# Kernel optimization log

Hardware: AMD Instinct MI355X
Metric: run time of the kernel (lower is better)

The kernel has to match this reference:

```python
import jax, jax.numpy as jnp
import numpy as np

B, T, D_MODEL, N_HEADS = 4, 2048, 1024, 16
D_K = D_MODEL // N_HEADS


def setup_inputs() -> dict:
    key = jax.random.key(0)
    kx, kq, kk, kv, ko = jax.random.split(key, 5)
    scale = 1.0 / np.sqrt(D_MODEL)  # ~ torch Linear init scale
    return {
        "x": jax.random.normal(kx, (B, T, D_MODEL), dtype=jnp.float32),
        "W_q": jax.random.uniform(kq, (D_MODEL, D_MODEL), jnp.float32, -scale, scale),
        "W_k": jax.random.uniform(kk, (D_MODEL, D_MODEL), jnp.float32, -scale, scale),
        "W_v": jax.random.uniform(kv, (D_MODEL, D_MODEL), jnp.float32, -scale, scale),
        "W_o": jax.random.uniform(ko, (D_MODEL, D_MODEL), jnp.float32, -scale, scale),
    }


def reference(x, W_q, W_k, W_v, W_o):
    b, t, _ = x.shape
    # nn.Linear(y) = y @ W.T ; split to (B, H, T, d_k)
    def split_heads(y):
        return y.reshape(b, t, N_HEADS, D_K).transpose(0, 2, 1, 3)

    Q = split_heads(x @ W_q.T)
    K = split_heads(x @ W_k.T)
    V = split_heads(x @ W_v.T)

    scores = jnp.einsum("bhqd,bhkd->bhqk", Q, K) / jnp.sqrt(jnp.float32(D_K))
    causal = jnp.triu(jnp.ones((t, t), dtype=bool), k=1)  # True = masked
    scores = jnp.where(causal, -jnp.inf, scores)
    weights = jax.nn.softmax(scores, axis=-1)
    out = jnp.einsum("bhqk,bhkd->bhqd", weights, V)
    out = out.transpose(0, 2, 1, 3).reshape(b, t, D_MODEL)
    return out @ W_o.T
```

## Files before the change

kernel.cpp:

```cpp
#include <hip/hip_runtime.h>

typedef __attribute__((ext_vector_type(8))) short s16x8;
typedef __attribute__((ext_vector_type(4))) float fx4;
typedef __attribute__((ext_vector_type(4))) int ix4;

#define B_SZ 4
#define T_SZ 2048
#define DM 1024
#define NH 16
#define DK 64
#define M_SZ (B_SZ * T_SZ)
#define NINF (-__builtin_inff())
#define QSCALE (0.125f * 1.44269504088896340736f)

__device__ __forceinline__ unsigned short f2bf(float f) {
    unsigned int u = __float_as_uint(f);
    unsigned int r = u + 0x7fffu + ((u >> 16) & 1u);
    return (unsigned short)(r >> 16);
}

__device__ __forceinline__ unsigned cvtpk(float lo, float hi) {
    unsigned r;
    asm("v_cvt_pk_bf16_f32 %0, %1, %2" : "=v"(r) : "v"(lo), "v"(hi));
    return r;
}

__device__ __forceinline__ void async16(const unsigned short* g, unsigned short* l) {
    __builtin_amdgcn_global_load_lds(
        (const __attribute__((address_space(1))) unsigned int*)g,
        (__attribute__((address_space(3))) unsigned int*)l, 16, 0, 0);
}

__global__ void cast_f32_bf16(const float* __restrict__ src, unsigned short* __restrict__ dst, int n) {
    int i = (blockIdx.x * blockDim.x + threadIdx.x) * 4;
    int stride = gridDim.x * blockDim.x * 4;
    for (; i + 3 < n; i += stride) {
        float4 v = *(const float4*)(src + i);
        ushort4 o;
        o.x = f2bf(v.x); o.y = f2bf(v.y); o.z = f2bf(v.z); o.w = f2bf(v.w);
        *(ushort4*)(dst + i) = o;
    }
}

__global__ void cast_w4(const float* __restrict__ s0, const float* __restrict__ s1,
                        const float* __restrict__ s2, const float* __restrict__ s3,
                        unsigned short* __restrict__ dst) {
    const float* s = (blockIdx.y == 0) ? s0 : (blockIdx.y == 1) ? s1 : (blockIdx.y == 2) ? s2 : s3;
    unsigned short* d = dst + (size_t)blockIdx.y * (DM * DM);
    int i = (blockIdx.x * blockDim.x + threadIdx.x) * 4;
    int stride = gridDim.x * blockDim.x * 4;
    for (; i + 3 < DM * DM; i += stride) {
        float4 v = *(const float4*)(s + i);
        ushort4 o;
        o.x = f2bf(v.x); o.y = f2bf(v.y); o.z = f2bf(v.z); o.w = f2bf(v.w);
        *(ushort4*)(d + i) = o;
    }
}

__global__ __launch_bounds__(512, 2) void gemm_qkv256(const unsigned short* __restrict__ A,
                                                      const unsigned short* __restrict__ W,
                                                      unsigned short* __restrict__ Qs,
                                                      unsigned short* __restrict__ Kb,
                                                      unsigned short* __restrict__ Vt) {
    __shared__ __align__(16) unsigned short S[49152];

    const int t = threadIdx.x;
    const int lane = t & 63, w = t >> 6;
    const int wm = w >> 2, wn = w & 3;
    const int lrow = lane & 15, lk = lane >> 4;
    const int bx = blockIdx.x;
    const int m0 = blockIdx.y * 128;
    const int K = DM;
    const int NKT = K / 64;

    fx4 acc[4][4] = {};

    const int srow = t >> 3;
    const int cs = (t & 7) ^ (srow & 7);
    const unsigned short* Ag = A + (long)(m0 + srow) * K + cs * 8;
    const unsigned short* Bg = W + (long)(bx * 256 + srow) * K + cs * 8;

    async16(Ag,           &S[t * 8]);
    async16(Ag + 64 * K,  &S[4096 + t * 8]);
    async16(Bg,           &S[16384 + t * 8]);
    async16(Bg + 64 * K,  &S[16384 + 4096 + t * 8]);
    async16(Bg + 128 * K, &S[16384 + 8192 + t * 8]);
    async16(Bg + 192 * K, &S[16384 + 12288 + t * 8]);
    asm volatile("s_waitcnt vmcnt(0)" ::: "memory");
    __syncthreads();

    for (int kt = 0; kt < NKT; ++kt) {
        const int cur = kt & 1;
        if (kt + 1 < NKT) {
            const int ko = (kt + 1) * 64;
            const int nbA = (cur ^ 1) * 8192;
            const int nbB = 16384 + (cur ^ 1) * 16384;
            async16(Ag + ko,           &S[nbA + t * 8]);
            async16(Ag + 64 * K + ko,  &S[nbA + 4096 + t * 8]);
            async16(Bg + ko,           &S[nbB + t * 8]);
            async16(Bg + 64 * K + ko,  &S[nbB + 4096 + t * 8]);
            async16(Bg + 128 * K + ko, &S[nbB + 8192 + t * 8]);
            async16(Bg + 192 * K + ko, &S[nbB + 12288 + t * 8]);
        }
        const unsigned short* Ab = &S[cur * 8192];
        const unsigned short* Bb = &S[16384 + cur * 16384];
#pragma unroll
        for (int kk = 0; kk < 2; ++kk) {
            const int sw = ((kk * 4 + lk) ^ (lrow & 7)) * 8;
            s16x8 af[4], bf[4];
#pragma unroll
            for (int mf = 0; mf < 4; ++mf)
                af[mf] = *(const s16x8*)&Ab[(wm * 64 + mf * 16 + lrow) * 64 + sw];
#pragma unroll
            for (int nf = 0; nf < 4; ++nf)
                bf[nf] = *(const s16x8*)&Bb[(wn * 64 + nf * 16 + lrow) * 64 + sw];
            __builtin_amdgcn_s_setprio(1);
#pragma unroll
            for (int mf = 0; mf < 4; ++mf)
#pragma unroll
                for (int nf = 0; nf < 4; ++nf)
                    acc[mf][nf] = __builtin_amdgcn_mfma_f32_16x16x32_bf16(af[mf], bf[nf], acc[mf][nf], 0, 0, 0);
            __builtin_amdgcn_s_setprio(0);
        }
        asm volatile("s_waitcnt vmcnt(0)" ::: "memory");
        __syncthreads();
    }

    const int which = bx >> 2;
    const int n0l = (bx & 3) * 256;
    if (which < 2) {
        unsigned short* dst = which ? Kb : Qs;
        const float sc = which ? 1.f : QSCALE;
#pragma unroll
        for (int mf = 0; mf < 4; ++mf)
#pragma unroll
            for (int nf = 0; nf < 4; ++nf)
#pragma unroll
                for (int r = 0; r < 4; ++r) {
                    int row = m0 + wm * 64 + mf * 16 + lk * 4 + r;
                    int col = n0l + wn * 64 + nf * 16 + lrow;
                    dst[(long)row * DM + col] = f2bf(acc[mf][nf][r] * sc);
                }
    } else {
#pragma unroll
        for (int mf = 0; mf < 4; ++mf)
#pragma unroll
            for (int nf = 0; nf < 4; ++nf) {
                const int cl = wn * 64 + nf * 16 + lrow;
                const int rl = wm * 64 + mf * 16 + lk * 4;
                ushort4 pk;
                pk.x = f2bf(acc[mf][nf][0]); pk.y = f2bf(acc[mf][nf][1]);
                pk.z = f2bf(acc[mf][nf][2]); pk.w = f2bf(acc[mf][nf][3]);
                *(ushort4*)&S[cl * 132 + rl] = pk;
            }
        __syncthreads();
        const int c = t >> 1, h2 = t & 1;
        unsigned short* vtp = Vt + (long)(n0l + c) * M_SZ + m0 + h2 * 64;
#pragma unroll
        for (int j = 0; j < 8; ++j) {
            union { struct { ushort4 a, b; } s; ix4 v; } u;
            u.s.a = *(const ushort4*)&S[c * 132 + h2 * 64 + j * 8];
            u.s.b = *(const ushort4*)&S[c * 132 + h2 * 64 + j * 8 + 4];
            *(ix4*)(vtp + j * 8) = u.v;
        }
    }
}

template<int OUT_BF16>
__global__ __launch_bounds__(256) void gemm_bt(const unsigned short* __restrict__ A,
                                               const unsigned short* __restrict__ Bw,
                                               void* __restrict__ Cout,
                                               int M, int N, int K, float scale) {
    __shared__ __align__(16) unsigned short As[2][128 * 32];
    __shared__ __align__(16) unsigned short Bs[2][128 * 32];

    const int t = threadIdx.x;
    const int lane = t & 63;
    const int w = t >> 6;
    const int wm = w >> 1, wn = w & 1;
    const int lrow = lane & 15, lk = lane >> 4;
    const int m0 = blockIdx.y * 128, n0 = blockIdx.x * 128;

    fx4 acc[4][4] = {};

    const int arow = t >> 2;
    const int acol = (t & 3) * 8;
    const unsigned short* Ag = A + (long)(m0 + arow) * K + acol;
    const unsigned short* Bg = Bw + (long)(n0 + arow) * K + acol;
    const int lds0 = t * 8;
    const int nk = K / 32;

    async16(Ag, &As[0][lds0]);
    async16(Ag + 64 * K, &As[0][lds0 + 64 * 32]);
    async16(Bg, &Bs[0][lds0]);
    async16(Bg + 64 * K, &Bs[0][lds0 + 64 * 32]);

    for (int kt = 0; kt < nk; ++kt) {
        const int cur = kt & 1;
        if (kt + 1 < nk) {
            const int ko = (kt + 1) * 32;
            async16(Ag + ko, &As[cur ^ 1][lds0]);
            async16(Ag + 64 * K + ko, &As[cur ^ 1][lds0 + 64 * 32]);
            async16(Bg + ko, &Bs[cur ^ 1][lds0]);
            async16(Bg + 64 * K + ko, &Bs[cur ^ 1][lds0 + 64 * 32]);
            asm volatile("s_waitcnt vmcnt(4)" ::: "memory");
        } else {
            asm volatile("s_waitcnt vmcnt(0)" ::: "memory");
        }
        __syncthreads();

        s16x8 af[4], bf[4];
#pragma unroll
        for (int i = 0; i < 4; ++i)
            af[i] = *(const s16x8*)&As[cur][(wm * 64 + i * 16 + lrow) * 32 + lk * 8];
#pragma unroll
        for (int i = 0; i < 4; ++i)
            bf[i] = *(const s16x8*)&Bs[cur][(wn * 64 + i * 16 + lrow) * 32 + lk * 8];
#pragma unroll
        for (int i = 0; i < 4; ++i)
#pragma unroll
            for (int j = 0; j < 4; ++j)
                acc[i][j] = __builtin_amdgcn_mfma_f32_16x16x32_bf16(af[i], bf[j], acc[i][j], 0, 0, 0);
        __syncthreads();
    }

#pragma unroll
    for (int i = 0; i < 4; ++i)
#pragma unroll
        for (int j = 0; j < 4; ++j)
#pragma unroll
            for (int r = 0; r < 4; ++r) {
                int row = m0 + wm * 64 + i * 16 + lk * 4 + r;
                int col = n0 + wn * 64 + j * 16 + lrow;
                float v = acc[i][j][r] * scale;
                if (OUT_BF16)
                    ((unsigned short*)Cout)[(long)row * N + col] = f2bf(v);
                else
                    ((float*)Cout)[(long)row * N + col] = v;
            }
}

__global__ __launch_bounds__(256, 4) void attn_kernel(const unsigned short* __restrict__ Q,
                                                      const unsigned short* __restrict__ Kb,
                                                      const unsigned short* __restrict__ Vt,
                                                      unsigned short* __restrict__ O) {
    __shared__ __align__(16) unsigned short Ks[2][64 * 64];
    __shared__ __align__(16) unsigned short Vs[2][64 * 64];
    __shared__ __align__(16) unsigned short Pl[4][16 * 72];

    const int t = threadIdx.x;
    const int lane = t & 63, w = t >> 6;
    const int lrow = lane & 15, lk = lane >> 4;
    const int hb = blockIdx.x;
    const int h = hb & 15, b = hb >> 4;
    const int qb = 15 - blockIdx.y;
    const int row0 = b * T_SZ;
    const int q0w = qb * 128 + w * 32;

    s16x8 qf[2][2];
#pragma unroll
    for (int hh = 0; hh < 2; ++hh) {
        const unsigned short* qp = Q + (long)(row0 + q0w + hh * 16 + lrow) * DM + h * DK + lk * 8;
        qf[hh][0] = *(const s16x8*)qp;
        qf[hh][1] = *(const s16x8*)(qp + 32);
    }

    fx4 acc[2][4] = {};
    float mrun[2] = {NINF, NINF}, lsum[2] = {0.f, 0.f};

    const int srow = t >> 3;
    const int chk = (t & 7) ^ (srow & 7);
    const unsigned short* Kg = Kb + (long)(row0 + srow) * DM + h * DK + chk * 8;
    const unsigned short* Vg = Vt + (long)(h * DK + srow) * M_SZ + row0 + chk * 8;
    unsigned short* Kl = &Ks[0][t * 8];
    unsigned short* Vl = &Vs[0][t * 8];

    const int nt = 2 * qb + 2;

    async16(Kg, Kl);
    async16(Kg + 32 * DM, Kl + 2048);
    async16(Vg, Vl);
    async16(Vg + 32 * (long)M_SZ, Vl + 2048);
    asm volatile("s_waitcnt vmcnt(0)" ::: "memory");
    __syncthreads();

    for (int kt = 0; kt < nt; ++kt) {
        const int cur = kt & 1;
        const bool pre = (kt + 1 < nt);
        if (pre) {
            const long koff = (long)(kt + 1) * 64 * DM;
            const int voff = (kt + 1) * 64;
            async16(Kg + koff, Kl + (cur ^ 1) * 4096);
            async16(Kg + koff + 32 * DM, Kl + (cur ^ 1) * 4096 + 2048);
            async16(Vg + voff, Vl + (cur ^ 1) * 4096);
            async16(Vg + voff + 32 * (long)M_SZ, Vl + (cur ^ 1) * 4096 + 2048);
        }
        const int kv0 = kt * 64;
        if (kv0 <= q0w + 31) {
            const char* ksb = (const char*)&Ks[cur][0];
            float p[2][4][4];
            float pm0 = NINF, pm1 = NINF;
#pragma unroll
            for (int sub = 0; sub < 4; ++sub) {
                const int kv0s = kv0 + sub * 16;
                if (kv0s <= q0w + 31) {
                    const int rb = (sub * 16 + lrow) << 7;
                    const int sw = (lrow & 7) << 4;
                    const s16x8 kf0 = *(const s16x8*)(ksb + (rb + ((lk * 16) ^ sw)));
                    const s16x8 kf1 = *(const s16x8*)(ksb + (rb + ((64 + lk * 16) ^ sw)));
                    fx4 s1 = {};
                    s1 = __builtin_amdgcn_mfma_f32_16x16x32_bf16(kf0, qf[1][0], s1, 0, 0, 0);
                    s1 = __builtin_amdgcn_mfma_f32_16x16x32_bf16(kf1, qf[1][1], s1, 0, 0, 0);
                    if (kv0s + 15 > q0w + 16) {
#pragma unroll
                        for (int r = 0; r < 4; ++r)
                            if (kv0s + lk * 4 + r > q0w + 16 + lrow) s1[r] = NINF;
                    }
#pragma unroll
                    for (int r = 0; r < 4; ++r) { p[1][sub][r] = s1[r]; pm1 = fmaxf(pm1, s1[r]); }
                    if (kv0s <= q0w + 15) {
                        fx4 s0 = {};
                        s0 = __builtin_amdgcn_mfma_f32_16x16x32_bf16(kf0, qf[0][0], s0, 0, 0, 0);
                        s0 = __builtin_amdgcn_mfma_f32_16x16x32_bf16(kf1, qf[0][1], s0, 0, 0, 0);
                        if (kv0s + 15 > q0w) {
#pragma unroll
                            for (int r = 0; r < 4; ++r)
                                if (kv0s + lk * 4 + r > q0w + lrow) s0[r] = NINF;
                        }
#pragma unroll
                        for (int r = 0; r < 4; ++r) { p[0][sub][r] = s0[r]; pm0 = fmaxf(pm0, s0[r]); }
                    } else {
#pragma unroll
                        for (int r = 0; r < 4; ++r) p[0][sub][r] = NINF;
                    }
                } else {
#pragma unroll
                    for (int r = 0; r < 4; ++r) { p[0][sub][r] = NINF; p[1][sub][r] = NINF; }
                }
            }
            float pmv[2] = {pm0, pm1};
#pragma unroll
            for (int hh = 0; hh < 2; ++hh) {
                float pm = pmv[hh];
                pm = fmaxf(pm, __shfl_xor(pm, 16));
                pm = fmaxf(pm, __shfl_xor(pm, 32));
                if (__any(pm > mrun[hh] + 8.f)) {
                    const float mnew = fmaxf(mrun[hh], pm);
                    const float sc = exp2f(mrun[hh] - mnew);
                    mrun[hh] = mnew;
                    lsum[hh] *= sc;
#pragma unroll
                    for (int r = 0; r < 4; ++r) {
                        const float scr = __shfl(sc, lk * 4 + r);
                        acc[hh][0][r] *= scr; acc[hh][1][r] *= scr;
                        acc[hh][2][r] *= scr; acc[hh][3][r] *= scr;
                    }
                }
                float ps = 0.f;
#pragma unroll
                for (int sub = 0; sub < 4; ++sub)
#pragma unroll
                    for (int r = 0; r < 4; ++r) {
                        const float pv = exp2f(p[hh][sub][r] - mrun[hh]);
                        p[hh][sub][r] = pv;
                        ps += pv;
                    }
                ps += __shfl_xor(ps, 16);
                ps += __shfl_xor(ps, 32);
                lsum[hh] += ps;
            }
            s16x8 pf[2][2];
#pragma unroll
            for (int hh = 0; hh < 2; ++hh) {
#pragma unroll
                for (int sub = 0; sub < 4; ++sub) {
                    uint2 pw;
                    pw.x = cvtpk(p[hh][sub][0], p[hh][sub][1]);
                    pw.y = cvtpk(p[hh][sub][2], p[hh][sub][3]);
                    *(uint2*)&Pl[w][lrow * 72 + sub * 16 + lk * 4] = pw;
                }
                pf[hh][0] = *(const s16x8*)&Pl[w][lrow * 72 + lk * 8];
                pf[hh][1] = *(const s16x8*)&Pl[w][lrow * 72 + 32 + lk * 8];
            }
#pragma unroll
            for (int s = 0; s < 2; ++s) {
                if (kv0 + s * 32 <= q0w + 31) {
                    const bool h0a = (kv0 + s * 32 <= q0w + 15);
#pragma unroll
                    for (int nf = 0; nf < 4; ++nf) {
                        const int d = nf * 16 + lrow;
                        const s16x8 vf = *(const s16x8*)&Vs[cur][d * 64 + (((s * 4 + lk) ^ (lrow & 7)) << 3)];
                        if (h0a)
                            acc[0][nf] = __builtin_amdgcn_mfma_f32_16x16x32_bf16(pf[0][s], vf, acc[0][nf], 0, 0, 0);
                        acc[1][nf] = __builtin_amdgcn_mfma_f32_16x16x32_bf16(pf[1][s], vf, acc[1][nf], 0, 0, 0);
                    }
                }
            }
        }
        asm volatile("s_waitcnt vmcnt(0)" ::: "memory");
        __syncthreads();
    }

#pragma unroll
    for (int hh = 0; hh < 2; ++hh) {
        float linv[4];
#pragma unroll
        for (int r = 0; r < 4; ++r) linv[r] = 1.f / __shfl(lsum[hh], lk * 4 + r);
        unsigned short* op = O + (long)(row0 + q0w + hh * 16) * DM + h * DK;
#pragma unroll
        for (int nf = 0; nf < 4; ++nf)
#pragma unroll
            for (int r = 0; r < 4; ++r)
                op[(long)(lk * 4 + r) * DM + nf * 16 + lrow] = f2bf(acc[hh][nf][r] * linv[r]);
    }
}

extern "C" void kernel_launch(void* const* d_in, const int* in_sizes, int n_in,
                              void* d_out, int out_size, void* d_ws, size_t ws_size,
                              hipStream_t stream) {
    const float* x  = (const float*)d_in[0];
    const float* Wq = (const float*)d_in[1];
    const float* Wk = (const float*)d_in[2];
    const float* Wv = (const float*)d_in[3];
    const float* Wo = (const float*)d_in[4];
    float* out = (float*)d_out;

    unsigned short* wsu = (unsigned short*)d_ws;
    unsigned short* xb  = wsu;
    unsigned short* wqb = xb + 8388608;
    unsigned short* wob = wqb + 3 * 1048576;
    unsigned short* Qs  = wob + 1048576;
    unsigned short* Ob  = Qs + 8388608;

    unsigned short* Kb = (unsigned short*)d_out;
    unsigned short* Vt = Kb + 8388608;

    cast_f32_bf16<<<2048, 256, 0, stream>>>(x, xb, M_SZ * DM);
    cast_w4<<<dim3(256, 4), 256, 0, stream>>>(Wq, Wk, Wv, Wo, wqb);

    gemm_qkv256<<<dim3(12, M_SZ / 128), 512, 0, stream>>>(xb, wqb, Qs, Kb, Vt);

    dim3 agrid(64, 16);
    attn_kernel<<<agrid, 256, 0, stream>>>(Qs, Kb, Vt, Ob);

    dim3 ggrid(DM / 128, M_SZ / 128);
    gemm_bt<0><<<ggrid, 256, 0, stream>>>(Ob, wob, out, M_SZ, DM, DM, 1.f);
}
```

Before: 198.9 us.

## Merge cast kernels, use 128x256 swizzled output GEMM, MFMA row sums in attention

Combines the x and weight cast kernels into one launch, cutting one kernel launch. Replaces the 128x128 output-projection GEMM with a 512-thread 128x256 tile that uses a K=64 step, XOR-swizzled LDS and s_setprio around the MFMA block, aiming for more reuse and fewer LDS bank conflicts. In attention, the softmax row-sum is computed by an MFMA against a ones vector instead of per-lane adds and shuffles, which adds MFMA work but removes the cross-lane reductions. The bf16 rounding of P now also enters the denominator, which slightly changes the numerics.

After: 201.0 us. Within noise of the previous version (+1.0%).

```diff
diff --git a/kernel.cpp b/kernel.cpp
--- a/kernel.cpp
+++ b/kernel.cpp
@@ -31,25 +31,23 @@
         (__attribute__((address_space(3))) unsigned int*)l, 16, 0, 0);
 }
 
-__global__ void cast_f32_bf16(const float* __restrict__ src, unsigned short* __restrict__ dst, int n) {
+__global__ void cast_all(const float* __restrict__ x,
+                         const float* __restrict__ s1, const float* __restrict__ s2,
+                         const float* __restrict__ s3, const float* __restrict__ s4,
+                         unsigned short* __restrict__ xb, unsigned short* __restrict__ wb) {
+    const int y = blockIdx.y;
+    const float* s;
+    unsigned short* d;
+    int n;
+    if (y == 0) { s = x; d = xb; n = M_SZ * DM; }
+    else {
+        s = (y == 1) ? s1 : (y == 2) ? s2 : (y == 3) ? s3 : s4;
+        d = wb + (size_t)(y - 1) * (DM * DM);
+        n = DM * DM;
+    }
     int i = (blockIdx.x * blockDim.x + threadIdx.x) * 4;
     int stride = gridDim.x * blockDim.x * 4;
     for (; i + 3 < n; i += stride) {
-        float4 v = *(const float4*)(src + i);
-        ushort4 o;
-        o.x = f2bf(v.x); o.y = f2bf(v.y); o.z = f2bf(v.z); o.w = f2bf(v.w);
-        *(ushort4*)(dst + i) = o;
-    }
-}
-
-__global__ void cast_w4(const float* __restrict__ s0, const float* __restrict__ s1,
-                        const float* __restrict__ s2, const float* __restrict__ s3,
-                        unsigned short* __restrict__ dst) {
-    const float* s = (blockIdx.y == 0) ? s0 : (blockIdx.y == 1) ? s1 : (blockIdx.y == 2) ? s2 : s3;
-    unsigned short* d = dst + (size_t)blockIdx.y * (DM * DM);
-    int i = (blockIdx.x * blockDim.x + threadIdx.x) * 4;
-    int stride = gridDim.x * blockDim.x * 4;
-    for (; i + 3 < DM * DM; i += stride) {
         float4 v = *(const float4*)(s + i);
         ushort4 o;
         o.x = f2bf(v.x); o.y = f2bf(v.y); o.z = f2bf(v.z); o.w = f2bf(v.w);
@@ -166,77 +164,82 @@
     }
 }
 
-template<int OUT_BF16>
-__global__ __launch_bounds__(256) void gemm_bt(const unsigned short* __restrict__ A,
-                                               const unsigned short* __restrict__ Bw,
-                                               void* __restrict__ Cout,
-                                               int M, int N, int K, float scale) {
-    __shared__ __align__(16) unsigned short As[2][128 * 32];
-    __shared__ __align__(16) unsigned short Bs[2][128 * 32];
+__global__ __launch_bounds__(512, 2) void gemm_out256(const unsigned short* __restrict__ A,
+                                                      const unsigned short* __restrict__ W,
+                                                      float* __restrict__ C) {
+    __shared__ __align__(16) unsigned short S[49152];
 
     const int t = threadIdx.x;
-    const int lane = t & 63;
-    const int w = t >> 6;
-    const int wm = w >> 1, wn = w & 1;
+    const int lane = t & 63, w = t >> 6;
+    const int wm = w >> 2, wn = w & 3;
     const int lrow = lane & 15, lk = lane >> 4;
-    const int m0 = blockIdx.y * 128, n0 = blockIdx.x * 128;
+    const int n0 = blockIdx.x * 256;
+    const int m0 = blockIdx.y * 128;
+    const int K = DM;
+    const int NKT = K / 64;
 
     fx4 acc[4][4] = {};
 
-    const int arow = t >> 2;
-    const int acol = (t & 3) * 8;
-    const unsigned short* Ag = A + (long)(m0 + arow) * K + acol;
-    const unsigned short* Bg = Bw + (long)(n0 + arow) * K + acol;
-    const int lds0 = t * 8;
-    const int nk = K / 32;
-
-    async16(Ag, &As[0][lds0]);
-    async16(Ag + 64 * K, &As[0][lds0 + 64 * 32]);
-    async16(Bg, &Bs[0][lds0]);
-    async16(Bg + 64 * K, &Bs[0][lds0 + 64 * 32]);
-
-    for (int kt = 0; kt < nk; ++kt) {
+    const int srow = t >> 3;
+    const int cs = (t & 7) ^ (srow & 7);
+    const unsigned short* Ag = A + (long)(m0 + srow) * K + cs * 8;
+    const unsigned short* Bg = W + (long)(n0 + srow) * K + cs * 8;
+
+    async16(Ag,           &S[t * 8]);
+    async16(Ag + 64 * K,  &S[4096 + t * 8]);
+    async16(Bg,           &S[16384 + t * 8]);
+    async16(Bg + 64 * K,  &S[16384 + 4096 + t * 8]);
+    async16(Bg + 128 * K, &S[16384 + 8192 + t * 8]);
+    async16(Bg + 192 * K, &S[16384 + 12288 + t * 8]);
+    asm volatile("s_waitcnt vmcnt(0)" ::: "memory");
+    __syncthreads();
+
+    for (int kt = 0; kt < NKT; ++kt) {
         const int cur = kt & 1;
-        if (kt + 1 < nk) {
-            const int ko = (kt + 1) * 32;
-            async16(Ag + ko, &As[cur ^ 1][lds0]);
-            async16(Ag + 64 * K + ko, &As[cur ^ 1][lds0 + 64 * 32]);
-            async16(Bg + ko, &Bs[cur ^ 1][lds0]);
-            async16(Bg + 64 * K + ko, &Bs[cur ^ 1][lds0 + 64 * 32]);
-            asm volatile("s_waitcnt vmcnt(4)" ::: "memory");
-        } else {
-            asm volatile("s_waitcnt vmcnt(0)" ::: "memory");
-        }
+        if (kt + 1 < NKT) {
+            const int ko = (kt + 1) * 64;
+            const int nbA = (cur ^ 1) * 8192;
+            const int nbB = 16384 + (cur ^ 1) * 16384;
+            async16(Ag + ko,           &S[nbA + t * 8]);
+            async16(Ag + 64 * K + ko,  &S[nbA + 4096 + t * 8]);
+            async16(Bg + ko,           &S[nbB + t * 8]);
+            async16(Bg + 64 * K + ko,  &S[nbB + 4096 + t * 8]);
+            async16(Bg + 128 * K + ko, &S[nbB + 8192 + t * 8]);
+            async16(Bg + 192 * K + ko, &S[nbB + 12288 + t * 8]);
+        }
+        const unsigned short* Ab = &S[cur * 8192];
+        const unsigned short* Bb = &S[16384 + cur * 16384];
+#pragma unroll
+        for (int kk = 0; kk < 2; ++kk) {
+            const int sw = ((kk * 4 + lk) ^ (lrow & 7)) * 8;
+            s16x8 af[4], bf[4];
+#pragma unroll
+            for (int mf = 0; mf < 4; ++mf)
+                af[mf] = *(const s16x8*)&Ab[(wm * 64 + mf * 16 + lrow) * 64 + sw];
+#pragma unroll
+            for (int nf = 0; nf < 4; ++nf)
+                bf[nf] = *(const s16x8*)&Bb[(wn * 64 + nf * 16 + lrow) * 64 + sw];
+            __builtin_amdgcn_s_setprio(1);
+#pragma unroll
+            for (int mf = 0; mf < 4; ++mf)
+#pragma unroll
+                for (int nf = 0; nf < 4; ++nf)
+                    acc[mf][nf] = __builtin_amdgcn_mfma_f32_16x16x32_bf16(af[mf], bf[nf], acc[mf][nf], 0, 0, 0);
+            __builtin_amdgcn_s_setprio(0);
+        }
+        asm volatile("s_waitcnt vmcnt(0)" ::: "memory");
         __syncthreads();
-
-        s16x8 af[4], bf[4];
-#pragma unroll
-        for (int i = 0; i < 4; ++i)
-            af[i] = *(const s16x8*)&As[cur][(wm * 64 + i * 16 + lrow) * 32 + lk * 8];
-#pragma unroll
-        for (int i = 0; i < 4; ++i)
-            bf[i] = *(const s16x8*)&Bs[cur][(wn * 64 + i * 16 + lrow) * 32 + lk * 8];
-#pragma unroll
-        for (int i = 0; i < 4; ++i)
-#pragma unroll
-            for (int j = 0; j < 4; ++j)
-                acc[i][j] = __builtin_amdgcn_mfma_f32_16x16x32_bf16(af[i], bf[j], acc[i][j], 0, 0, 0);
-        __syncthreads();
-    }
-
-#pragma unroll
-    for (int i = 0; i < 4; ++i)
-#pragma unroll
-        for (int j = 0; j < 4; ++j)
+    }
+
+#pragma unroll
+    for (int mf = 0; mf < 4; ++mf)
+#pragma unroll
+        for (int nf = 0; nf < 4; ++nf)
 #pragma unroll
             for (int r = 0; r < 4; ++r) {
-                int row = m0 + wm * 64 + i * 16 + lk * 4 + r;
-                int col = n0 + wn * 64 + j * 16 + lrow;
-                float v = acc[i][j][r] * scale;
-                if (OUT_BF16)
-                    ((unsigned short*)Cout)[(long)row * N + col] = f2bf(v);
-                else
-                    ((float*)Cout)[(long)row * N + col] = v;
+                int row = m0 + wm * 64 + mf * 16 + lk * 4 + r;
+                int col = n0 + wn * 64 + nf * 16 + lrow;
+                C[(long)row * DM + col] = acc[mf][nf][r];
             }
 }
 
@@ -265,8 +268,12 @@
         qf[hh][1] = *(const s16x8*)(qp + 32);
     }
 
+    const short onebf = (short)0x3F80;
+    const s16x8 ones = {onebf, onebf, onebf, onebf, onebf, onebf, onebf, onebf};
+
     fx4 acc[2][4] = {};
-    float mrun[2] = {NINF, NINF}, lsum[2] = {0.f, 0.f};
+    fx4 suml[2] = {};
+    float mrun[2] = {NINF, NINF};
 
     const int srow = t >> 3;
     const int chk = (t & 7) ^ (srow & 7);
@@ -348,26 +355,19 @@
                     const float mnew = fmaxf(mrun[hh], pm);
                     const float sc = exp2f(mrun[hh] - mnew);
                     mrun[hh] = mnew;
-                    lsum[hh] *= sc;
 #pragma unroll
                     for (int r = 0; r < 4; ++r) {
                         const float scr = __shfl(sc, lk * 4 + r);
                         acc[hh][0][r] *= scr; acc[hh][1][r] *= scr;
                         acc[hh][2][r] *= scr; acc[hh][3][r] *= scr;
+                        suml[hh][r] *= scr;
                     }
                 }
-                float ps = 0.f;
 #pragma unroll
                 for (int sub = 0; sub < 4; ++sub)
 #pragma unroll
-                    for (int r = 0; r < 4; ++r) {
-                        const float pv = exp2f(p[hh][sub][r] - mrun[hh]);
-                        p[hh][sub][r] = pv;
-                        ps += pv;
-                    }
-                ps += __shfl_xor(ps, 16);
-                ps += __shfl_xor(ps, 32);
-                lsum[hh] += ps;
+                    for (int r = 0; r < 4; ++r)
+                        p[hh][sub][r] = exp2f(p[hh][sub][r] - mrun[hh]);
             }
             s16x8 pf[2][2];
 #pragma unroll
@@ -386,6 +386,9 @@
             for (int s = 0; s < 2; ++s) {
                 if (kv0 + s * 32 <= q0w + 31) {
                     const bool h0a = (kv0 + s * 32 <= q0w + 15);
+                    if (h0a)
+                        suml[0] = __builtin_amdgcn_mfma_f32_16x16x32_bf16(pf[0][s], ones, suml[0], 0, 0, 0);
+                    suml[1] = __builtin_amdgcn_mfma_f32_16x16x32_bf16(pf[1][s], ones, suml[1], 0, 0, 0);
 #pragma unroll
                     for (int nf = 0; nf < 4; ++nf) {
                         const int d = nf * 16 + lrow;
@@ -405,7 +408,7 @@
     for (int hh = 0; hh < 2; ++hh) {
         float linv[4];
 #pragma unroll
-        for (int r = 0; r < 4; ++r) linv[r] = 1.f / __shfl(lsum[hh], lk * 4 + r);
+        for (int r = 0; r < 4; ++r) linv[r] = 1.f / suml[hh][r];
         unsigned short* op = O + (long)(row0 + q0w + hh * 16) * DM + h * DK;
 #pragma unroll
         for (int nf = 0; nf < 4; ++nf)
@@ -435,14 +438,12 @@
     unsigned short* Kb = (unsigned short*)d_out;
     unsigned short* Vt = Kb + 8388608;
 
-    cast_f32_bf16<<<2048, 256, 0, stream>>>(x, xb, M_SZ * DM);
-    cast_w4<<<dim3(256, 4), 256, 0, stream>>>(Wq, Wk, Wv, Wo, wqb);
+    cast_all<<<dim3(512, 5), 256, 0, stream>>>(x, Wq, Wk, Wv, Wo, xb, wqb);
 
     gemm_qkv256<<<dim3(12, M_SZ / 128), 512, 0, stream>>>(xb, wqb, Qs, Kb, Vt);
 
     dim3 agrid(64, 16);
     attn_kernel<<<agrid, 256, 0, stream>>>(Qs, Kb, Vt, Ob);
 
-    dim3 ggrid(DM / 128, M_SZ / 128);
-    gemm_bt<0><<<ggrid, 256, 0, stream>>>(Ob, wob, out, M_SZ, DM, DM, 1.f);
-}
+    gemm_out256<<<dim3(DM / 256, M_SZ / 128), 512, 0, stream>>>(Ob, wob, out);
+}
```
